# Optimization experiments

Hardware: AMD Instinct MI355X
Metric: run time of the kernel (lower is better)

## Reference

```python
import jax, jax.numpy as jnp
import numpy as np

LN_EPS = 1e-12

def setup_inputs() -> dict:
    key = jax.random.key(0)
    k1, k2 = jax.random.split(key)
    batch, seq_len, hidden, conv_size = 32, 2048, 512, 64
    input_tensor = jax.random.normal(k1, (batch, seq_len, hidden), dtype=jnp.float32)
    conv_weight = jax.random.normal(k2, (1, conv_size, hidden), dtype=jnp.float32) * 0.02
    gamma = jnp.ones((hidden,), dtype=jnp.float32)
    beta = jnp.zeros((hidden,), dtype=jnp.float32)
    return {"input_tensor": input_tensor, "conv_weight": conv_weight, "gamma": gamma, "beta": beta}

def reference(input_tensor, conv_weight, gamma, beta):
    # input_tensor: [B, S, H]; conv_weight: [1, K, H] (K << S)
    seq_len = input_tensor.shape[1]
    conv_size = conv_weight.shape[1]
    # FFT-based circular depthwise convolution along the sequence axis
    x_f = jnp.fft.rfft(input_tensor, axis=1, norm='ortho')            # [B, S//2+1, H] complex
    w_pad = jnp.pad(conv_weight, ((0, 0), (0, seq_len - conv_size), (0, 0)))  # zero-pad filter to S
    w_f = jnp.fft.rfft(w_pad, axis=1, norm='ortho')                   # [1, S//2+1, H]
    y = jnp.fft.irfft(x_f * w_f, n=seq_len, axis=1, norm='ortho')     # [B, S, H]
    # dropout is identity at inference; residual + LayerNorm(eps=1e-12)
    h = y + input_tensor
    mean = jnp.mean(h, axis=-1, keepdims=True)
    var = jnp.mean(jnp.square(h - mean), axis=-1, keepdims=True)
    return gamma * (h - mean) * jax.lax.rsqrt(var + LN_EPS) + beta
```

## Files before the change

### kernel.cpp

```cpp
#include <hip/hip_runtime.h>

#define S_LEN 2048
#define HDIM  512
#define KSZ   64
#define S_T   128
#define PH    16
#define INV_SQRT_S 0.02209708691207961f

struct Smem {
    float  lh[PH][HDIM];
    float2 part[PH][33];
    float2 stats[PH];
};

__device__ __forceinline__ void lds_barrier() {
    asm volatile("s_waitcnt lgkmcnt(0)\n\ts_barrier" ::: "memory");
}

template <int OFF>
__device__ __forceinline__ void conv_phase(const float* __restrict__ xb, int sbase, int h,
                                           const float (&wr)[KSZ], float (&xw)[KSZ],
                                           float (&xp)[PH], float (&hv)[PH], Smem* sm)
{
#pragma unroll
    for (int j = 0; j < PH; ++j) {
        const float xcur = xp[j];
        xp[j] = xb[((sbase + j + PH) & (S_LEN - 1)) * HDIM + h];

        float y0 = 0.f, y1 = 0.f, y2 = 0.f, y3 = 0.f;
#pragma unroll
        for (int k = 1; k <= KSZ - 7; k += 4) {
            y0 = fmaf(wr[k],     xw[(OFF + j - k)     & 63], y0);
            y1 = fmaf(wr[k + 1], xw[(OFF + j - k - 1) & 63], y1);
            y2 = fmaf(wr[k + 2], xw[(OFF + j - k - 2) & 63], y2);
            y3 = fmaf(wr[k + 3], xw[(OFF + j - k - 3) & 63], y3);
        }
        y0 = fmaf(wr[61], xw[(OFF + j - 61) & 63], y0);
        y1 = fmaf(wr[62], xw[(OFF + j - 62) & 63], y1);
        y2 = fmaf(wr[63], xw[(OFF + j - 63) & 63], y2);

        const float hval = fmaf(INV_SQRT_S, fmaf(wr[0], xcur, (y0 + y1) + (y2 + y3)), xcur);
        xw[(OFF + j) & 63] = xcur;
        hv[j] = hval;
        sm->lh[j][h] = hval;
    }
}

__device__ __forceinline__ void ln_phase(int sbase, int h, const float (&hv)[PH],
                                         float gm, float bt, float* __restrict__ ob, Smem* sm)
{
    lds_barrier();

    const int r = h >> 5, c = h & 31;
    float s1 = 0.f, q1 = 0.f;
#pragma unroll
    for (int m = 0; m < 16; ++m) {
        const float v = sm->lh[r][c + (m << 5)];
        s1 += v;
        q1 = fmaf(v, v, q1);
    }
    sm->part[r][c] = make_float2(s1, q1);
    lds_barrier();

    if (h < 64) {
        const int rr = h >> 2, q = h & 3;
        float ts = 0.f, tq = 0.f;
#pragma unroll
        for (int i = 0; i < 8; ++i) {
            const float2 p = sm->part[rr][q * 8 + i];
            ts += p.x; tq += p.y;
        }
        ts += __shfl_xor(ts, 1, 64); tq += __shfl_xor(tq, 1, 64);
        ts += __shfl_xor(ts, 2, 64); tq += __shfl_xor(tq, 2, 64);
        if (q == 0) {
            const float mean = ts * (1.0f / 512.0f);
            const float var  = fmaf(tq, 1.0f / 512.0f, -mean * mean);
            sm->stats[rr] = make_float2(mean, rsqrtf(var + 1e-12f));
        }
    }
    lds_barrier();

#pragma unroll
    for (int j = 0; j < PH; ++j) {
        const float2 st = sm->stats[j];
        ob[(sbase + j) * HDIM + h] = fmaf((hv[j] - st.x) * st.y, gm, bt);
    }
}

__global__ __launch_bounds__(512, 2)
void fconv_ln(const float* __restrict__ x, const float* __restrict__ w,
              const float* __restrict__ gamma, const float* __restrict__ beta,
              float* __restrict__ out)
{
    __shared__ Smem sm;
    const int h  = threadIdx.x;
    const int b  = blockIdx.x >> 4;
    const int s0 = (blockIdx.x & 15) * S_T;

    const float* xb = x   + (size_t)b * S_LEN * HDIM;
    float*       ob = out + (size_t)b * S_LEN * HDIM;

    float wr[KSZ];
#pragma unroll
    for (int k = 0; k < KSZ; ++k) wr[k] = w[k * HDIM + h];
    const float gm = gamma[h], bt = beta[h];

    float xw[KSZ];
#pragma unroll
    for (int d = 1; d < KSZ; ++d)
        xw[KSZ - d] = xb[((s0 - d) & (S_LEN - 1)) * HDIM + h];
    xw[0] = 0.f;

    float xp[PH], hv[PH];
#pragma unroll
    for (int j = 0; j < PH; ++j) xp[j] = xb[(s0 + j) * HDIM + h];

    for (int grp = 0; grp < S_T / 64; ++grp) {
        const int base = s0 + grp * 64;
        conv_phase<0 >(xb, base +  0, h, wr, xw, xp, hv, &sm); ln_phase(base +  0, h, hv, gm, bt, ob, &sm);
        conv_phase<16>(xb, base + 16, h, wr, xw, xp, hv, &sm); ln_phase(base + 16, h, hv, gm, bt, ob, &sm);
        conv_phase<32>(xb, base + 32, h, wr, xw, xp, hv, &sm); ln_phase(base + 32, h, hv, gm, bt, ob, &sm);
        conv_phase<48>(xb, base + 48, h, wr, xw, xp, hv, &sm); ln_phase(base + 48, h, hv, gm, bt, ob, &sm);
    }
}

extern "C" void kernel_launch(void* const* d_in, const int* in_sizes, int n_in,
                              void* d_out, int out_size, void* d_ws, size_t ws_size,
                              hipStream_t stream) {
    const float* x  = (const float*)d_in[0];
    const float* w  = (const float*)d_in[1];
    const float* g  = (const float*)d_in[2];
    const float* b  = (const float*)d_in[3];
    float* o        = (float*)d_out;

    (void)in_sizes; (void)n_in; (void)out_size; (void)d_ws; (void)ws_size;
    fconv_ln<<<dim3(32 * (S_LEN / S_T)), dim3(HDIM), 0, stream>>>(x, w, g, b, o);
}
```

Measured before the change: 267.1 us.

## Split depthwise conv taps across two thread halves and combine partials in LDS

Each block now uses 1024 threads. Each half of the block computes 32 of the 64 filter taps for the same channel and writes a partial sum into its own LDS buffer. The LayerNorm phase adds the two partials, stores h in a shared buffer, reduces statistics with 64-wide partials, and each half then writes 8 of the 16 rows. This halves the per-thread register arrays for weights and window, which is meant to raise occupancy and parallelism. The cost is extra LDS traffic, a larger shared footprint, and duplicated global reads of x by both halves.

```diff
diff --git a/kernel.cpp b/kernel.cpp
--- a/kernel.cpp
+++ b/kernel.cpp
@@ -3,13 +3,15 @@
 #define S_LEN 2048
 #define HDIM  512
 #define KSZ   64
+#define HALFK 32
 #define S_T   128
 #define PH    16
 #define INV_SQRT_S 0.02209708691207961f
 
 struct Smem {
-    float  lh[PH][HDIM];
-    float2 part[PH][33];
+    float  pbuf[2][PH][HDIM];
+    float  hbuf[PH][HDIM];
+    float2 part[PH][64];
     float2 stats[PH];
 };
 
@@ -18,60 +20,59 @@
 }
 
 template <int OFF>
-__device__ __forceinline__ void conv_phase(const float* __restrict__ xb, int sbase, int h,
-                                           const float (&wr)[KSZ], float (&xw)[KSZ],
-                                           float (&xp)[PH], float (&hv)[PH], Smem* sm)
+__device__ __forceinline__ void conv_phase(const float* __restrict__ xb, int mbase, int h, float res,
+                                           const float (&wr)[HALFK], float (&xw)[HALFK],
+                                           float (&xp)[4], float* __restrict__ pdst)
 {
 #pragma unroll
-    for (int j = 0; j < PH; ++j) {
-        const float xcur = xp[j];
-        xp[j] = xb[((sbase + j + PH) & (S_LEN - 1)) * HDIM + h];
+    for (int j2 = 0; j2 < PH; ++j2) {
+        const float xcur = xp[j2 & 3];
+        xp[j2 & 3] = xb[((mbase + j2 + 4) & (S_LEN - 1)) * HDIM + h];
 
+        xw[(OFF + j2) & 31] = xcur;
         float y0 = 0.f, y1 = 0.f, y2 = 0.f, y3 = 0.f;
 #pragma unroll
-        for (int k = 1; k <= KSZ - 7; k += 4) {
-            y0 = fmaf(wr[k],     xw[(OFF + j - k)     & 63], y0);
-            y1 = fmaf(wr[k + 1], xw[(OFF + j - k - 1) & 63], y1);
-            y2 = fmaf(wr[k + 2], xw[(OFF + j - k - 2) & 63], y2);
-            y3 = fmaf(wr[k + 3], xw[(OFF + j - k - 3) & 63], y3);
+        for (int i = 0; i < HALFK; i += 4) {
+            y0 = fmaf(wr[i],     xw[(OFF + j2 - i)     & 31], y0);
+            y1 = fmaf(wr[i + 1], xw[(OFF + j2 - i - 1) & 31], y1);
+            y2 = fmaf(wr[i + 2], xw[(OFF + j2 - i - 2) & 31], y2);
+            y3 = fmaf(wr[i + 3], xw[(OFF + j2 - i - 3) & 31], y3);
         }
-        y0 = fmaf(wr[61], xw[(OFF + j - 61) & 63], y0);
-        y1 = fmaf(wr[62], xw[(OFF + j - 62) & 63], y1);
-        y2 = fmaf(wr[63], xw[(OFF + j - 63) & 63], y2);
-
-        const float hval = fmaf(INV_SQRT_S, fmaf(wr[0], xcur, (y0 + y1) + (y2 + y3)), xcur);
-        xw[(OFF + j) & 63] = xcur;
-        hv[j] = hval;
-        sm->lh[j][h] = hval;
+        const float y = (y0 + y1) + (y2 + y3);
+        pdst[j2 * HDIM] = fmaf(res, xcur, INV_SQRT_S * y);
     }
 }
 
-__device__ __forceinline__ void ln_phase(int sbase, int h, const float (&hv)[PH],
-                                         float gm, float bt, float* __restrict__ ob, Smem* sm)
+__device__ __forceinline__ void ln_phase(int srow0, int tid, int h, float gm, float bt,
+                                         float* __restrict__ ob, Smem* sm)
 {
     lds_barrier();
 
-    const int r = h >> 5, c = h & 31;
+    const int r = tid >> 6, c = tid & 63;
     float s1 = 0.f, q1 = 0.f;
 #pragma unroll
-    for (int m = 0; m < 16; ++m) {
-        const float v = sm->lh[r][c + (m << 5)];
+    for (int m = 0; m < 8; ++m) {
+        const int col = c + (m << 6);
+        const float v = sm->pbuf[0][r][col] + sm->pbuf[1][r][col];
+        sm->hbuf[r][col] = v;
         s1 += v;
         q1 = fmaf(v, v, q1);
     }
     sm->part[r][c] = make_float2(s1, q1);
     lds_barrier();
 
-    if (h < 64) {
-        const int rr = h >> 2, q = h & 3;
+    if (tid < 256) {
+        const int rr = tid >> 4, q = tid & 15;
         float ts = 0.f, tq = 0.f;
 #pragma unroll
-        for (int i = 0; i < 8; ++i) {
-            const float2 p = sm->part[rr][q * 8 + i];
+        for (int i = 0; i < 4; ++i) {
+            const float2 p = sm->part[rr][q * 4 + i];
             ts += p.x; tq += p.y;
         }
         ts += __shfl_xor(ts, 1, 64); tq += __shfl_xor(tq, 1, 64);
         ts += __shfl_xor(ts, 2, 64); tq += __shfl_xor(tq, 2, 64);
+        ts += __shfl_xor(ts, 4, 64); tq += __shfl_xor(tq, 4, 64);
+        ts += __shfl_xor(ts, 8, 64); tq += __shfl_xor(tq, 8, 64);
         if (q == 0) {
             const float mean = ts * (1.0f / 512.0f);
             const float var  = fmaf(tq, 1.0f / 512.0f, -mean * mean);
@@ -80,47 +81,60 @@
     }
     lds_barrier();
 
+    const int half = tid >> 9;
 #pragma unroll
-    for (int j = 0; j < PH; ++j) {
-        const float2 st = sm->stats[j];
-        ob[(sbase + j) * HDIM + h] = fmaf((hv[j] - st.x) * st.y, gm, bt);
+    for (int i = 0; i < 8; ++i) {
+        const int rr = half * 8 + i;
+        const float2 st = sm->stats[rr];
+        const float v = sm->hbuf[rr][h];
+        ob[(srow0 + rr) * HDIM + h] = fmaf((v - st.x) * st.y, gm, bt);
     }
 }
 
-__global__ __launch_bounds__(512, 2)
+__global__ __launch_bounds__(1024, 4)
 void fconv_ln(const float* __restrict__ x, const float* __restrict__ w,
               const float* __restrict__ gamma, const float* __restrict__ beta,
               float* __restrict__ out)
 {
     __shared__ Smem sm;
-    const int h  = threadIdx.x;
-    const int b  = blockIdx.x >> 4;
-    const int s0 = (blockIdx.x & 15) * S_T;
+    const int tid    = threadIdx.x;
+    const int h      = tid & (HDIM - 1);
+    const int half   = tid >> 9;
+    const int halfsh = half << 5;
+    const int b      = blockIdx.x >> 4;
+    const int s0     = (blockIdx.x & 15) * S_T;
 
     const float* xb = x   + (size_t)b * S_LEN * HDIM;
     float*       ob = out + (size_t)b * S_LEN * HDIM;
 
-    float wr[KSZ];
+    float wr[HALFK];
 #pragma unroll
-    for (int k = 0; k < KSZ; ++k) wr[k] = w[k * HDIM + h];
-    const float gm = gamma[h], bt = beta[h];
+    for (int i = 0; i < HALFK; ++i) wr[i] = w[(halfsh + i) * HDIM + h];
+    const float gm  = gamma[h], bt = beta[h];
+    const float res = half ? 0.0f : 1.0f;
 
-    float xw[KSZ];
+    const int m0 = s0 - halfsh;
+
+    float xw[HALFK];
 #pragma unroll
-    for (int d = 1; d < KSZ; ++d)
-        xw[KSZ - d] = xb[((s0 - d) & (S_LEN - 1)) * HDIM + h];
+    for (int d = 1; d < HALFK; ++d)
+        xw[(HALFK - d) & 31] = xb[((m0 - d) & (S_LEN - 1)) * HDIM + h];
     xw[0] = 0.f;
 
-    float xp[PH], hv[PH];
+    float xp[4];
 #pragma unroll
-    for (int j = 0; j < PH; ++j) xp[j] = xb[(s0 + j) * HDIM + h];
+    for (int j = 0; j < 4; ++j)
+        xp[j] = xb[((m0 + j) & (S_LEN - 1)) * HDIM + h];
 
-    for (int grp = 0; grp < S_T / 64; ++grp) {
-        const int base = s0 + grp * 64;
-        conv_phase<0 >(xb, base +  0, h, wr, xw, xp, hv, &sm); ln_phase(base +  0, h, hv, gm, bt, ob, &sm);
-        conv_phase<16>(xb, base + 16, h, wr, xw, xp, hv, &sm); ln_phase(base + 16, h, hv, gm, bt, ob, &sm);
-        conv_phase<32>(xb, base + 32, h, wr, xw, xp, hv, &sm); ln_phase(base + 32, h, hv, gm, bt, ob, &sm);
-        conv_phase<48>(xb, base + 48, h, wr, xw, xp, hv, &sm); ln_phase(base + 48, h, hv, gm, bt, ob, &sm);
+    float* pdst = &sm.pbuf[half][0][h];
+
+#pragma unroll 1
+    for (int g = 0; g < S_T / (2 * PH); ++g) {
+        const int jb = g * 2 * PH;
+        conv_phase<0> (xb, m0 + jb,      h, res, wr, xw, xp, pdst);
+        ln_phase(s0 + jb,      tid, h, gm, bt, ob, &sm);
+        conv_phase<16>(xb, m0 + jb + PH, h, res, wr, xw, xp, pdst);
+        ln_phase(s0 + jb + PH, tid, h, gm, bt, ob, &sm);
     }
 }
 
@@ -134,5 +148,5 @@
     float* o        = (float*)d_out;
 
     (void)in_sizes; (void)n_in; (void)out_size; (void)d_ws; (void)ws_size;
-    fconv_ln<<<dim3(32 * (S_LEN / S_T)), dim3(HDIM), 0, stream>>>(x, w, g, b, o);
+    fconv_ln<<<dim3(32 * (S_LEN / S_T)), dim3(1024), 0, stream>>>(x, w, g, b, o);
 }
```

Result: slower. 284.3 us (+6.4%).
